# Optimization experiments

Hardware: AMD Instinct MI355X
Metric: run time of the kernel (lower is better)

Reference implementation:

```python
import jax, jax.numpy as jnp
import numpy as np

D_K = 64
SCALE = D_K ** (-0.5)
B, H, S = 2, 16, 2048


def setup_inputs() -> dict:
    key = jax.random.key(0)
    kq, kk, kv = jax.random.split(key, 3)
    q = jax.random.normal(kq, (B, H, S, D_K), dtype=jnp.float32)
    k = jax.random.normal(kk, (B, H, S, D_K), dtype=jnp.float32)
    v = jax.random.normal(kv, (B, H, S, D_K), dtype=jnp.float32)
    # causal mask: True means masked (matches torch masked_fill semantics)
    mask = jnp.triu(jnp.ones((S, S), dtype=bool), k=1)[None, None]  # [1,1,S,S]
    return {"q": q, "k": k, "v": v, "mask": mask}


def reference(q, k, v, mask) -> jnp.ndarray:
    # scores = q @ k^T  -> [B,H,S,S]
    scores = jnp.einsum("bhqd,bhkd->bhqk", q, k)
    # masked_fill(mask, -inf), then scale (as written in the source),
    # then softmax over the key axis. -inf * scale stays -inf.
    scores = jnp.where(mask, -jnp.inf, scores)
    attn = jax.nn.softmax(SCALE * scores, axis=-1)
    return jnp.einsum("bhqk,bhkd->bhqd", attn, v)
```

## Files before the change

kernel.cpp:

```cpp
#include <hip/hip_runtime.h>
#include <hip/hip_bf16.h>
#include <math.h>


constexpr int S  = 2048;
constexpr int D  = 64;
constexpr int BH = 32;
constexpr float SCALE = 0.125f;
constexpr float LOG2E = 1.4426950408889634f;
constexpr float QPRE  = SCALE * LOG2E;
constexpr int PSTR = 72;

typedef __attribute__((ext_vector_type(8))) short bf16x8;
typedef __attribute__((ext_vector_type(4))) short bf16x4;
typedef __attribute__((ext_vector_type(4))) float f32x4;

#if __has_builtin(__builtin_amdgcn_mfma_f32_16x16x16bf16_1k)
#define HAS_MFMA_1K 1
#else
#define HAS_MFMA_1K 0
#endif

#if __has_builtin(__builtin_amdgcn_exp2f)
#define EXP2F(x) __builtin_amdgcn_exp2f(x)
#else
#define EXP2F(x) exp2f(x)
#endif

__device__ __forceinline__ short f2bf(float x) {
    union { __hip_bfloat16 b; short s; } u; u.b = __float2bfloat16(x); return u.s;
}

__device__ __forceinline__ void gload_lds16(const void* g, void* lds) {
    __builtin_amdgcn_global_load_lds(
        (const __attribute__((address_space(1))) unsigned int*)g,
        (__attribute__((address_space(3))) unsigned int*)lds, 16, 0, 0);
}

__global__ __launch_bounds__(256) void preconv_25993142075924(
    const float* __restrict__ Kg, const float* __restrict__ Vg,
    short* __restrict__ Kb, short* __restrict__ VT)
{
    const int kt = blockIdx.x, bh = blockIdx.y, tid = threadIdx.x;
    __shared__ float lt[64 * 65];
    const float* kp = Kg + (size_t)bh * S * D;
    const float* vp = Vg + (size_t)bh * S * D;
    short* kb = Kb + (size_t)bh * S * D;
    short* vt = VT + (size_t)bh * D * S;
    #pragma unroll
    for (int e = 0; e < 4; ++e) {
        int idx = (tid + e * 256) * 4;
        int r = idx >> 6, c = idx & 63;
        f32x4 k4 = *(const f32x4*)(kp + (size_t)(kt * 64 + r) * D + c);
        bf16x4 kb4;
        kb4[0] = f2bf(k4[0]); kb4[1] = f2bf(k4[1]);
        kb4[2] = f2bf(k4[2]); kb4[3] = f2bf(k4[3]);
        *(bf16x4*)(kb + (size_t)(kt * 64 + r) * D + c) = kb4;
        f32x4 v4 = *(const f32x4*)(vp + (size_t)(kt * 64 + r) * D + c);
        lt[(c + 0) * 65 + r] = v4[0];
        lt[(c + 1) * 65 + r] = v4[1];
        lt[(c + 2) * 65 + r] = v4[2];
        lt[(c + 3) * 65 + r] = v4[3];
    }
    __syncthreads();
    #pragma unroll
    for (int e = 0; e < 2; ++e) {
        int tt = tid + e * 256;
        int d  = tt >> 3;
        int j0 = (tt & 7) * 8;
        bf16x8 o;
        #pragma unroll
        for (int jj = 0; jj < 8; ++jj)
            o[jj] = f2bf(lt[d * 65 + j0 + jj]);
        *(bf16x8*)(vt + (size_t)d * S + kt * 64 + j0) = o;
    }
}

__global__ __launch_bounds__(256, 2) void attn_fwd_v9_25993142075924(
    const float* __restrict__ Qg, const short* __restrict__ Kb,
    const short* __restrict__ VT, float* __restrict__ Og)
{
    const int bh  = blockIdx.x;
    const int yy  = blockIdx.y;
    const int qb  = (yy < 8) ? (15 - yy) : (yy - 8);
    const int tid = threadIdx.x;
    const int wv  = tid >> 6;
    const int ln  = tid & 63;
    const int c16 = ln & 15;
    const int qd  = ln >> 4;

    const int w0    = qb * 128 + wv * 32;
    const int nkt   = 2 * qb + 2;
    const int mask0 = w0 >> 6;

    __shared__ __align__(16) short lk[2][64 * 64];
    __shared__ __align__(16) short lv[2][64 * 64];
#if !HAS_MFMA_1K
    __shared__ __align__(16) short lp[4 * 16 * PSTR];
    short* lpw = lp + wv * 16 * PSTR;
#endif

    const float* qp = Qg + (size_t)bh * S * D;
    const short* kp = Kb + (size_t)bh * S * D;
    const short* vp = VT + (size_t)bh * D * S;
    float*       op = Og + (size_t)bh * S * D;

    const int srow0 = wv * 16 + (ln >> 3);
    const int sgrp0 = (ln & 7) ^ (srow0 & 7);
    const int srow1 = srow0 + 8;
    const int sgrp1 = (ln & 7) ^ (srow1 & 7);

    bf16x8 qf[2][2];
    #pragma unroll
    for (int sp = 0; sp < 2; ++sp) {
        const float* src = qp + (size_t)(w0 + sp * 16 + c16) * D + qd * 8;
        #pragma unroll
        for (int khf = 0; khf < 2; ++khf) {
            f32x4 a = *(const f32x4*)(src + khf * 32);
            f32x4 b = *(const f32x4*)(src + khf * 32 + 4);
            bf16x8 f;
            f[0] = f2bf(a[0] * QPRE); f[1] = f2bf(a[1] * QPRE);
            f[2] = f2bf(a[2] * QPRE); f[3] = f2bf(a[3] * QPRE);
            f[4] = f2bf(b[0] * QPRE); f[5] = f2bf(b[1] * QPRE);
            f[6] = f2bf(b[2] * QPRE); f[7] = f2bf(b[3] * QPRE);
            qf[sp][khf] = f;
        }
    }

    f32x4 oacc[2][4] = {{{0,0,0,0},{0,0,0,0},{0,0,0,0},{0,0,0,0}},
                        {{0,0,0,0},{0,0,0,0},{0,0,0,0},{0,0,0,0}}};
    float lsum[2] = {0.f, 0.f};

    gload_lds16(kp + (size_t)srow0 * D + sgrp0 * 8, &lk[0][(wv * 16 + 0) * 64]);
    gload_lds16(vp + (size_t)srow0 * S + sgrp0 * 8, &lv[0][(wv * 16 + 0) * 64]);
    gload_lds16(kp + (size_t)srow1 * D + sgrp1 * 8, &lk[0][(wv * 16 + 8) * 64]);
    gload_lds16(vp + (size_t)srow1 * S + sgrp1 * 8, &lv[0][(wv * 16 + 8) * 64]);
    __syncthreads();

    for (int kt = 0; kt < nkt; ++kt) {
        const int cur = kt & 1;
        if (kt + 1 < nkt) {
            const int nxt = cur ^ 1;
            const size_t kb0 = (size_t)(kt + 1) * 64;
            gload_lds16(kp + (kb0 + srow0) * D + sgrp0 * 8, &lk[nxt][(wv * 16 + 0) * 64]);
            gload_lds16(vp + (size_t)srow0 * S + kb0 + sgrp0 * 8, &lv[nxt][(wv * 16 + 0) * 64]);
            gload_lds16(kp + (kb0 + srow1) * D + sgrp1 * 8, &lk[nxt][(wv * 16 + 8) * 64]);
            gload_lds16(vp + (size_t)srow1 * S + kb0 + sgrp1 * 8, &lv[nxt][(wv * 16 + 8) * 64]);
        }

        if (kt * 64 <= w0 + 31) {
#if HAS_MFMA_1K
            bf16x4 vf[4][4];
            #pragma unroll
            for (int dt = 0; dt < 4; ++dt) {
                const int row = dt * 16 + c16;
                #pragma unroll
                for (int nt = 0; nt < 4; ++nt) {
                    const int gl = nt * 2 + (qd >> 1);
                    const int gp = gl ^ (c16 & 7);
                    vf[dt][nt] = *(const bf16x4*)&lv[cur][row * 64 + gp * 8 + (qd & 1) * 4];
                }
            }
#endif

            float t0[4][4], t1[4][4];
            #pragma unroll
            for (int nt = 0; nt < 4; ++nt) {
                const int row = nt * 16 + c16;
                f32x4 a0 = {0,0,0,0}, a1 = {0,0,0,0};
                #pragma unroll
                for (int khf = 0; khf < 2; ++khf) {
                    const int g = (khf * 4 + qd) ^ (row & 7);
                    bf16x8 kf = *(const bf16x8*)&lk[cur][row * 64 + g * 8];
                    a0 = __builtin_amdgcn_mfma_f32_16x16x32_bf16(kf, qf[0][khf], a0, 0, 0, 0);
                    a1 = __builtin_amdgcn_mfma_f32_16x16x32_bf16(kf, qf[1][khf], a1, 0, 0, 0);
                }
                #pragma unroll
                for (int r = 0; r < 4; ++r) { t0[nt][r] = a0[r]; t1[nt][r] = a1[r]; }
            }

            if (kt >= mask0) {
                #pragma unroll
                for (int nt = 0; nt < 4; ++nt) {
                    #pragma unroll
                    for (int r = 0; r < 4; ++r) {
                        int key = kt * 64 + nt * 16 + qd * 4 + r;
                        if (key > w0 + c16)      t0[nt][r] = -INFINITY;
                        if (key > w0 + 16 + c16) t1[nt][r] = -INFINITY;
                    }
                }
            }

            #pragma unroll
            for (int sp = 0; sp < 2; ++sp) {
                float (&t)[4][4] = sp ? t1 : t0;
#if HAS_MFMA_1K
                #pragma unroll
                for (int nt = 0; nt < 4; ++nt) {
                    bf16x4 pf;
                    #pragma unroll
                    for (int r = 0; r < 4; ++r) {
                        float pv = EXP2F(t[nt][r]);
                        lsum[sp] += pv;
                        pf[r] = f2bf(pv);
                    }
                    #pragma unroll
                    for (int dt = 0; dt < 4; ++dt)
                        oacc[sp][dt] = __builtin_amdgcn_mfma_f32_16x16x16bf16_1k(
                            vf[dt][nt], pf, oacc[sp][dt], 0, 0, 0);
                }
#else
                #pragma unroll
                for (int nt = 0; nt < 4; ++nt)
                    #pragma unroll
                    for (int r = 0; r < 4; ++r) {
                        float pv = EXP2F(t[nt][r]);
                        lsum[sp] += pv;
                        lpw[c16 * PSTR + nt * 16 + qd * 4 + r] = f2bf(pv);
                    }
                bf16x8 pf2[2];
                #pragma unroll
                for (int khf = 0; khf < 2; ++khf)
                    pf2[khf] = *(const bf16x8*)&lpw[c16 * PSTR + khf * 32 + qd * 8];
                #pragma unroll
                for (int dt = 0; dt < 4; ++dt) {
                    const int row = dt * 16 + c16;
                    #pragma unroll
                    for (int khf = 0; khf < 2; ++khf) {
                        const int g = (khf * 4 + qd) ^ (row & 7);
                        bf16x8 vf8 = *(const bf16x8*)&lv[cur][row * 64 + g * 8];
                        oacc[sp][dt] = __builtin_amdgcn_mfma_f32_16x16x32_bf16(
                            vf8, pf2[khf], oacc[sp][dt], 0, 0, 0);
                    }
                }
#endif
            }
        }

        __syncthreads();
    }

    #pragma unroll
    for (int sp = 0; sp < 2; ++sp) {
        float s2 = lsum[sp];
        s2 += __shfl_xor(s2, 16);
        s2 += __shfl_xor(s2, 32);
        const float inv = 1.0f / s2;
        float* dst = op + (size_t)(w0 + sp * 16 + c16) * D;
        #pragma unroll
        for (int dt = 0; dt < 4; ++dt) {
            f32x4 o;
            o[0] = oacc[sp][dt][0] * inv; o[1] = oacc[sp][dt][1] * inv;
            o[2] = oacc[sp][dt][2] * inv; o[3] = oacc[sp][dt][3] * inv;
            *(f32x4*)(dst + dt * 16 + qd * 4) = o;
        }
    }
}

__global__ __launch_bounds__(256) void attn_fwd_v1_25993142075924(
    const float* __restrict__ Qg, const float* __restrict__ Kg,
    const float* __restrict__ Vg, float* __restrict__ Og)
{
    constexpr int KSTR = 72;
    constexpr int BQ = 64, BK = 64;
    const int qt  = blockIdx.x;
    const int bh  = blockIdx.y;
    const int tid = threadIdx.x;
    const int wv  = tid >> 6;
    const int ln  = tid & 63;
    const int c16 = ln & 15;
    const int qd  = ln >> 4;

    __shared__ __align__(16) __hip_bfloat16 lk [BK][KSTR];
    __shared__ __align__(16) __hip_bfloat16 lvt[D ][KSTR];
    __shared__ __align__(16) __hip_bfloat16 lp [4][16][KSTR];

    const size_t hoff = (size_t)bh * S * D;
    const float* qp = Qg + hoff;
    const float* kp = Kg + hoff;
    const float* vp = Vg + hoff;
    float*       op = Og + hoff;
    const int q0 = qt * BQ;

    bf16x8 qf[2];
    {
        const float* src = qp + (size_t)(q0 + wv*16 + c16) * D + qd*8;
        #pragma unroll
        for (int kh = 0; kh < 2; ++kh) {
            f32x4 a = *(const f32x4*)(src + kh*32);
            f32x4 b = *(const f32x4*)(src + kh*32 + 4);
            bf16x8 f;
            f[0]=f2bf(a[0]*QPRE); f[1]=f2bf(a[1]*QPRE); f[2]=f2bf(a[2]*QPRE); f[3]=f2bf(a[3]*QPRE);
            f[4]=f2bf(b[0]*QPRE); f[5]=f2bf(b[1]*QPRE); f[6]=f2bf(b[2]*QPRE); f[7]=f2bf(b[3]*QPRE);
            qf[kh] = f;
        }
    }

    f32x4 oacc[4] = {{0,0,0,0},{0,0,0,0},{0,0,0,0},{0,0,0,0}};
    float mrun[4] = {-INFINITY,-INFINITY,-INFINITY,-INFINITY};
    float lrun[4] = {0.f,0.f,0.f,0.f};

    const int nkt = qt + 1;
    for (int kt = 0; kt < nkt; ++kt) {
        __syncthreads();
        #pragma unroll
        for (int e = 0; e < 4; ++e) {
            int idx = (tid + e*256) * 4;
            int row = idx >> 6, col = idx & 63;
            f32x4 k4 = *(const f32x4*)(kp + (size_t)(kt*BK + row)*D + col);
            bf16x4 kb;
            kb[0]=f2bf(k4[0]); kb[1]=f2bf(k4[1]); kb[2]=f2bf(k4[2]); kb[3]=f2bf(k4[3]);
            *(bf16x4*)&lk[row][col] = kb;
            f32x4 v4 = *(const f32x4*)(vp + (size_t)(kt*BK + row)*D + col);
            lvt[col+0][row] = __float2bfloat16(v4[0]);
            lvt[col+1][row] = __float2bfloat16(v4[1]);
            lvt[col+2][row] = __float2bfloat16(v4[2]);
            lvt[col+3][row] = __float2bfloat16(v4[3]);
        }
        __syncthreads();

        float t[4][4];
        #pragma unroll
        for (int nt = 0; nt < 4; ++nt) {
            f32x4 acc = {0,0,0,0};
            #pragma unroll
            for (int kh = 0; kh < 2; ++kh) {
                bf16x8 kf = *(const bf16x8*)&lk[nt*16 + c16][kh*32 + qd*8];
                acc = __builtin_amdgcn_mfma_f32_16x16x32_bf16(qf[kh], kf, acc, 0, 0, 0);
            }
            #pragma unroll
            for (int r = 0; r < 4; ++r) t[nt][r] = acc[r];
        }
        if (kt == nkt - 1) {
            #pragma unroll
            for (int nt = 0; nt < 4; ++nt) {
                int j = kt*BK + nt*16 + c16;
                #pragma unroll
                for (int r = 0; r < 4; ++r)
                    if (j > q0 + wv*16 + qd*4 + r) t[nt][r] = -INFINITY;
            }
        }

        float pval[4][4];
        #pragma unroll
        for (int r = 0; r < 4; ++r) {
            float tm = fmaxf(fmaxf(t[0][r], t[1][r]), fmaxf(t[2][r], t[3][r]));
            tm = fmaxf(tm, __shfl_xor(tm, 1));
            tm = fmaxf(tm, __shfl_xor(tm, 2));
            tm = fmaxf(tm, __shfl_xor(tm, 4));
            tm = fmaxf(tm, __shfl_xor(tm, 8));
            float mnew  = fmaxf(mrun[r], tm);
            float alpha = exp2f(mrun[r] - mnew);
            mrun[r] = mnew;
            float rs = 0.f;
            #pragma unroll
            for (int nt = 0; nt < 4; ++nt) {
                float pv = exp2f(t[nt][r] - mnew);
                pval[nt][r] = pv;
                rs += pv;
            }
            rs += __shfl_xor(rs, 1);
            rs += __shfl_xor(rs, 2);
            rs += __shfl_xor(rs, 4);
            rs += __shfl_xor(rs, 8);
            lrun[r] = lrun[r] * alpha + rs;
            #pragma unroll
            for (int dt = 0; dt < 4; ++dt) oacc[dt][r] *= alpha;
        }

        #pragma unroll
        for (int nt = 0; nt < 4; ++nt)
            #pragma unroll
            for (int r = 0; r < 4; ++r)
                lp[wv][qd*4 + r][nt*16 + c16] = __float2bfloat16(pval[nt][r]);
        bf16x8 pf[2];
        #pragma unroll
        for (int kh = 0; kh < 2; ++kh)
            pf[kh] = *(const bf16x8*)&lp[wv][c16][kh*32 + qd*8];

        #pragma unroll
        for (int dt = 0; dt < 4; ++dt) {
            #pragma unroll
            for (int kh = 0; kh < 2; ++kh) {
                bf16x8 vf = *(const bf16x8*)&lvt[dt*16 + c16][kh*32 + qd*8];
                oacc[dt] = __builtin_amdgcn_mfma_f32_16x16x32_bf16(pf[kh], vf, oacc[dt], 0, 0, 0);
            }
        }
    }

    #pragma unroll
    for (int r = 0; r < 4; ++r) {
        float inv = 1.0f / lrun[r];
        float* dst = op + (size_t)(q0 + wv*16 + qd*4 + r) * D;
        #pragma unroll
        for (int dt = 0; dt < 4; ++dt)
            dst[dt*16 + c16] = oacc[dt][r] * inv;
    }
}

extern "C" void kernel_launch(void* const* d_in, const int* in_sizes, int n_in,
                              void* d_out, int out_size, void* d_ws, size_t ws_size,
                              hipStream_t stream) {
    const float* q = (const float*)d_in[0];
    const float* k = (const float*)d_in[1];
    const float* v = (const float*)d_in[2];
    float* out = (float*)d_out;
    const size_t elems = (size_t)BH * S * D;
    const size_t need  = 2 * elems * sizeof(short);
    if (ws_size >= need) {
        short* Kb = (short*)d_ws;
        short* VT = Kb + elems;
        preconv_25993142075924<<<dim3(S / 64, BH), 256, 0, stream>>>(k, v, Kb, VT);
        attn_fwd_v9_25993142075924<<<dim3(BH, 16), 256, 0, stream>>>(q, Kb, VT, out);
    } else {
        attn_fwd_v1_25993142075924<<<dim3(S / 64, BH), 256, 0, stream>>>(q, k, v, out);
    }
}
```

Before: 142.1 us.

## Shrink attention blocks to 64 queries with two waves and finer causal tiling

The attention kernel now uses 128-thread blocks covering 64 query rows instead of 256 threads covering 128 rows. The grid doubles to 32 query blocks per head, launched largest-first. Each block loads exactly qb+1 key tiles, so waves no longer skip fully masked tiles and masking happens only on the diagonal tile. K fragments are preloaded into registers and the MFMA calls are interleaved. This aims to balance causal work more finely and raise occupancy, at the cost of each K/V tile being reloaded by twice as many blocks and each thread issuing more staging loads.

```diff
diff --git a/kernel.cpp b/kernel.cpp
--- a/kernel.cpp
+++ b/kernel.cpp
@@ -76,27 +76,25 @@
     }
 }
 
-__global__ __launch_bounds__(256, 2) void attn_fwd_v9_25993142075924(
+__global__ __launch_bounds__(128, 4) void attn_fwd_v16_25993142075924(
     const float* __restrict__ Qg, const short* __restrict__ Kb,
     const short* __restrict__ VT, float* __restrict__ Og)
 {
     const int bh  = blockIdx.x;
-    const int yy  = blockIdx.y;
-    const int qb  = (yy < 8) ? (15 - yy) : (yy - 8);
+    const int qb  = 31 - (int)blockIdx.y;
     const int tid = threadIdx.x;
     const int wv  = tid >> 6;
     const int ln  = tid & 63;
     const int c16 = ln & 15;
     const int qd  = ln >> 4;
 
-    const int w0    = qb * 128 + wv * 32;
-    const int nkt   = 2 * qb + 2;
-    const int mask0 = w0 >> 6;
+    const int w0  = qb * 64 + wv * 32;
+    const int nkt = qb + 1;
 
     __shared__ __align__(16) short lk[2][64 * 64];
     __shared__ __align__(16) short lv[2][64 * 64];
 #if !HAS_MFMA_1K
-    __shared__ __align__(16) short lp[4 * 16 * PSTR];
+    __shared__ __align__(16) short lp[2 * 16 * PSTR];
     short* lpw = lp + wv * 16 * PSTR;
 #endif
 
@@ -105,10 +103,18 @@
     const short* vp = VT + (size_t)bh * D * S;
     float*       op = Og + (size_t)bh * S * D;
 
-    const int srow0 = wv * 16 + (ln >> 3);
-    const int sgrp0 = (ln & 7) ^ (srow0 & 7);
-    const int srow1 = srow0 + 8;
-    const int sgrp1 = (ln & 7) ^ (srow1 & 7);
+    #define STAGE(t, buf)                                                          \
+        do {                                                                       \
+            _Pragma("unroll")                                                      \
+            for (int e = 0; e < 4; ++e) {                                          \
+                const int sr = wv * 32 + e * 8 + (ln >> 3);                        \
+                const int sg = (ln & 7) ^ (sr & 7);                                \
+                gload_lds16(kp + ((size_t)(t) * 64 + sr) * D + sg * 8,             \
+                            &lk[buf][(wv * 32 + e * 8) * 64]);                     \
+                gload_lds16(vp + (size_t)sr * S + (t) * 64 + sg * 8,               \
+                            &lv[buf][(wv * 32 + e * 8) * 64]);                     \
+            }                                                                      \
+        } while (0)
 
     bf16x8 qf[2][2];
     #pragma unroll
@@ -131,114 +137,108 @@
                         {{0,0,0,0},{0,0,0,0},{0,0,0,0},{0,0,0,0}}};
     float lsum[2] = {0.f, 0.f};
 
-    gload_lds16(kp + (size_t)srow0 * D + sgrp0 * 8, &lk[0][(wv * 16 + 0) * 64]);
-    gload_lds16(vp + (size_t)srow0 * S + sgrp0 * 8, &lv[0][(wv * 16 + 0) * 64]);
-    gload_lds16(kp + (size_t)srow1 * D + sgrp1 * 8, &lk[0][(wv * 16 + 8) * 64]);
-    gload_lds16(vp + (size_t)srow1 * S + sgrp1 * 8, &lv[0][(wv * 16 + 8) * 64]);
+    STAGE(0, 0);
     __syncthreads();
 
     for (int kt = 0; kt < nkt; ++kt) {
         const int cur = kt & 1;
-        if (kt + 1 < nkt) {
-            const int nxt = cur ^ 1;
-            const size_t kb0 = (size_t)(kt + 1) * 64;
-            gload_lds16(kp + (kb0 + srow0) * D + sgrp0 * 8, &lk[nxt][(wv * 16 + 0) * 64]);
-            gload_lds16(vp + (size_t)srow0 * S + kb0 + sgrp0 * 8, &lv[nxt][(wv * 16 + 0) * 64]);
-            gload_lds16(kp + (kb0 + srow1) * D + sgrp1 * 8, &lk[nxt][(wv * 16 + 8) * 64]);
-            gload_lds16(vp + (size_t)srow1 * S + kb0 + sgrp1 * 8, &lv[nxt][(wv * 16 + 8) * 64]);
-        }
-
-        if (kt * 64 <= w0 + 31) {
+        if (kt + 1 < nkt) STAGE(kt + 1, cur ^ 1);
+
 #if HAS_MFMA_1K
-            bf16x4 vf[4][4];
+        bf16x4 vf[4][4];
+        #pragma unroll
+        for (int dt = 0; dt < 4; ++dt) {
+            const int row = dt * 16 + c16;
+            #pragma unroll
+            for (int nt = 0; nt < 4; ++nt) {
+                const int gl = nt * 2 + (qd >> 1);
+                const int gp = gl ^ (c16 & 7);
+                vf[dt][nt] = *(const bf16x4*)&lv[cur][row * 64 + gp * 8 + (qd & 1) * 4];
+            }
+        }
+#endif
+
+        bf16x8 kf0[4], kf1[4];
+        #pragma unroll
+        for (int nt = 0; nt < 4; ++nt) {
+            const int row = nt * 16 + c16;
+            kf0[nt] = *(const bf16x8*)&lk[cur][row * 64 + ((0 + qd) ^ (row & 7)) * 8];
+            kf1[nt] = *(const bf16x8*)&lk[cur][row * 64 + ((4 + qd) ^ (row & 7)) * 8];
+        }
+
+        float t0[4][4], t1[4][4];
+        #pragma unroll
+        for (int nt = 0; nt < 4; ++nt) {
+            f32x4 a0 = {0,0,0,0}, a1 = {0,0,0,0};
+            a0 = __builtin_amdgcn_mfma_f32_16x16x32_bf16(kf0[nt], qf[0][0], a0, 0, 0, 0);
+            a1 = __builtin_amdgcn_mfma_f32_16x16x32_bf16(kf0[nt], qf[1][0], a1, 0, 0, 0);
+            a0 = __builtin_amdgcn_mfma_f32_16x16x32_bf16(kf1[nt], qf[0][1], a0, 0, 0, 0);
+            a1 = __builtin_amdgcn_mfma_f32_16x16x32_bf16(kf1[nt], qf[1][1], a1, 0, 0, 0);
+            #pragma unroll
+            for (int r = 0; r < 4; ++r) { t0[nt][r] = a0[r]; t1[nt][r] = a1[r]; }
+        }
+
+        if (kt == qb) {
+            #pragma unroll
+            for (int nt = 0; nt < 4; ++nt) {
+                #pragma unroll
+                for (int r = 0; r < 4; ++r) {
+                    int key = kt * 64 + nt * 16 + qd * 4 + r;
+                    if (key > w0 + c16)      t0[nt][r] = -INFINITY;
+                    if (key > w0 + 16 + c16) t1[nt][r] = -INFINITY;
+                }
+            }
+        }
+
+        #pragma unroll
+        for (int sp = 0; sp < 2; ++sp) {
+            float (&t)[4][4] = sp ? t1 : t0;
+#if HAS_MFMA_1K
+            #pragma unroll
+            for (int nt = 0; nt < 4; ++nt) {
+                float p0 = EXP2F(t[nt][0]);
+                float p1 = EXP2F(t[nt][1]);
+                float p2 = EXP2F(t[nt][2]);
+                float p3 = EXP2F(t[nt][3]);
+                lsum[sp] += (p0 + p1) + (p2 + p3);
+                bf16x4 pf;
+                pf[0] = f2bf(p0); pf[1] = f2bf(p1);
+                pf[2] = f2bf(p2); pf[3] = f2bf(p3);
+                #pragma unroll
+                for (int dt = 0; dt < 4; ++dt)
+                    oacc[sp][dt] = __builtin_amdgcn_mfma_f32_16x16x16bf16_1k(
+                        vf[dt][nt], pf, oacc[sp][dt], 0, 0, 0);
+            }
+#else
+            #pragma unroll
+            for (int nt = 0; nt < 4; ++nt)
+                #pragma unroll
+                for (int r = 0; r < 4; ++r) {
+                    float pv = EXP2F(t[nt][r]);
+                    lsum[sp] += pv;
+                    lpw[c16 * PSTR + nt * 16 + qd * 4 + r] = f2bf(pv);
+                }
+            bf16x8 pf2[2];
+            #pragma unroll
+            for (int khf = 0; khf < 2; ++khf)
+                pf2[khf] = *(const bf16x8*)&lpw[c16 * PSTR + khf * 32 + qd * 8];
             #pragma unroll
             for (int dt = 0; dt < 4; ++dt) {
                 const int row = dt * 16 + c16;
                 #pragma unroll
-                for (int nt = 0; nt < 4; ++nt) {
-                    const int gl = nt * 2 + (qd >> 1);
-                    const int gp = gl ^ (c16 & 7);
-                    vf[dt][nt] = *(const bf16x4*)&lv[cur][row * 64 + gp * 8 + (qd & 1) * 4];
-                }
-            }
-#endif
-
-            float t0[4][4], t1[4][4];
-            #pragma unroll
-            for (int nt = 0; nt < 4; ++nt) {
-                const int row = nt * 16 + c16;
-                f32x4 a0 = {0,0,0,0}, a1 = {0,0,0,0};
-                #pragma unroll
                 for (int khf = 0; khf < 2; ++khf) {
                     const int g = (khf * 4 + qd) ^ (row & 7);
-                    bf16x8 kf = *(const bf16x8*)&lk[cur][row * 64 + g * 8];
-                    a0 = __builtin_amdgcn_mfma_f32_16x16x32_bf16(kf, qf[0][khf], a0, 0, 0, 0);
-                    a1 = __builtin_amdgcn_mfma_f32_16x16x32_bf16(kf, qf[1][khf], a1, 0, 0, 0);
+                    bf16x8 vf8 = *(const bf16x8*)&lv[cur][row * 64 + g * 8];
+                    oacc[sp][dt] = __builtin_amdgcn_mfma_f32_16x16x32_bf16(
+                        vf8, pf2[khf], oacc[sp][dt], 0, 0, 0);
                 }
-                #pragma unroll
-                for (int r = 0; r < 4; ++r) { t0[nt][r] = a0[r]; t1[nt][r] = a1[r]; }
-            }
-
-            if (kt >= mask0) {
-                #pragma unroll
-                for (int nt = 0; nt < 4; ++nt) {
-                    #pragma unroll
-                    for (int r = 0; r < 4; ++r) {
-                        int key = kt * 64 + nt * 16 + qd * 4 + r;
-                        if (key > w0 + c16)      t0[nt][r] = -INFINITY;
-                        if (key > w0 + 16 + c16) t1[nt][r] = -INFINITY;
-                    }
-                }
-            }
-
-            #pragma unroll
-            for (int sp = 0; sp < 2; ++sp) {
-                float (&t)[4][4] = sp ? t1 : t0;
-#if HAS_MFMA_1K
-                #pragma unroll
-                for (int nt = 0; nt < 4; ++nt) {
-                    bf16x4 pf;
-                    #pragma unroll
-                    for (int r = 0; r < 4; ++r) {
-                        float pv = EXP2F(t[nt][r]);
-                        lsum[sp] += pv;
-                        pf[r] = f2bf(pv);
-                    }
-                    #pragma unroll
-                    for (int dt = 0; dt < 4; ++dt)
-                        oacc[sp][dt] = __builtin_amdgcn_mfma_f32_16x16x16bf16_1k(
-                            vf[dt][nt], pf, oacc[sp][dt], 0, 0, 0);
-                }
-#else
-                #pragma unroll
-                for (int nt = 0; nt < 4; ++nt)
-                    #pragma unroll
-                    for (int r = 0; r < 4; ++r) {
-                        float pv = EXP2F(t[nt][r]);
-                        lsum[sp] += pv;
-                        lpw[c16 * PSTR + nt * 16 + qd * 4 + r] = f2bf(pv);
-                    }
-                bf16x8 pf2[2];
-                #pragma unroll
-                for (int khf = 0; khf < 2; ++khf)
-                    pf2[khf] = *(const bf16x8*)&lpw[c16 * PSTR + khf * 32 + qd * 8];
-                #pragma unroll
-                for (int dt = 0; dt < 4; ++dt) {
-                    const int row = dt * 16 + c16;
-                    #pragma unroll
-                    for (int khf = 0; khf < 2; ++khf) {
-                        const int g = (khf * 4 + qd) ^ (row & 7);
-                        bf16x8 vf8 = *(const bf16x8*)&lv[cur][row * 64 + g * 8];
-                        oacc[sp][dt] = __builtin_amdgcn_mfma_f32_16x16x32_bf16(
-                            vf8, pf2[khf], oacc[sp][dt], 0, 0, 0);
-                    }
-                }
+            }
 #endif
-            }
         }
 
         __syncthreads();
     }
+    #undef STAGE
 
     #pragma unroll
     for (int sp = 0; sp < 2; ++sp) {
@@ -411,7 +411,7 @@
         short* Kb = (short*)d_ws;
         short* VT = Kb + elems;
         preconv_25993142075924<<<dim3(S / 64, BH), 256, 0, stream>>>(k, v, Kb, VT);
-        attn_fwd_v9_25993142075924<<<dim3(BH, 16), 256, 0, stream>>>(q, Kb, VT, out);
+        attn_fwd_v16_25993142075924<<<dim3(BH, 32), 128, 0, stream>>>(q, Kb, VT, out);
     } else {
         attn_fwd_v1_25993142075924<<<dim3(S / 64, BH), 256, 0, stream>>>(q, k, v, out);
     }
```

After: 144.2 us. About the same (+1.5%).
